# Performance work log

Measured on AMD Instinct MI355X. Metric: run time of the kernel, lower is better.

Reference implementation:

```python
import jax, jax.numpy as jnp
import numpy as np

N = 10000      # nodes
E = 320000     # edges (avg degree 32)
H = 128        # hidden_channels
G = 50         # num_gaussians
NF = 128       # num_filters
L = 6          # num_interactions
CUTOFF = 10.0


def ssp(x):
    # ShiftedSoftplus: softplus(x) - log(2)
    return jax.nn.softplus(x) - jnp.log(2.0).astype(x.dtype)


def setup_inputs() -> dict:
    key = jax.random.key(0)
    ks = jax.random.split(key, 16)
    s = 0.05
    return {
        "z": jax.random.normal(ks[0], (N, H), jnp.float32),
        "pos": jax.random.normal(ks[1], (N, 3), jnp.float32) * 3.0,
        "edge_index": jax.random.randint(ks[2], (2, E), 0, N, dtype=jnp.int64),
        # per-layer stacked parameters (PyTorch Linear convention: y = x @ W.T + b)
        "mlp1_w": jax.random.normal(ks[3], (L, NF, G), jnp.float32) * s,
        "mlp1_b": jnp.zeros((L, NF), jnp.float32),
        "mlp2_w": jax.random.normal(ks[4], (L, NF, NF), jnp.float32) * s,
        "mlp2_b": jnp.zeros((L, NF), jnp.float32),
        "lin1_w": jax.random.normal(ks[5], (L, NF, H), jnp.float32) * s,   # no bias
        "lin2_w": jax.random.normal(ks[6], (L, H, NF), jnp.float32) * s,
        "lin2_b": jnp.zeros((L, H), jnp.float32),
        "lin_w": jax.random.normal(ks[7], (L, H, H), jnp.float32) * s,
        "lin_b": jnp.zeros((L, H), jnp.float32),
        "coord_w": jax.random.normal(ks[8], (L, 1, G + 2 * H), jnp.float32) * s,
        "coord_b": jnp.zeros((L, 1), jnp.float32),
    }


def reference(z, pos, edge_index, mlp1_w, mlp1_b, mlp2_w, mlp2_b,
              lin1_w, lin2_w, lin2_b, lin_w, lin_b, coord_w, coord_b):
    row, col = edge_index[0], edge_index[1]
    # edge distances from INITIAL positions (computed once, as in torch code)
    edge_weight = jnp.linalg.norm(pos[row] - pos[col], axis=-1)          # [E]
    offset = jnp.linspace(0.0, CUTOFF, G).astype(pos.dtype)              # [G]
    coeff = -0.5 / (offset[1] - offset[0]) ** 2
    edge_attr = jnp.exp(coeff * (edge_weight[:, None] - offset[None, :]) ** 2)  # [E,G]
    C = 0.5 * (jnp.cos(edge_weight * jnp.pi / CUTOFF) + 1.0)             # [E] cosine cutoff
    ones_e = jnp.ones((E,), pos.dtype)
    h = z
    for l in range(L):
        # ---- coordinate update (uses current pos and current h) ----
        feat = jnp.concatenate([edge_attr, h[row], h[col]], axis=-1)     # [E, G+2H]
        cw = feat @ coord_w[l].T + coord_b[l]                            # [E,1]
        aggr = (pos[row] - pos[col]) * cw                                # [E,3]
        sums = jax.ops.segment_sum(aggr, row, num_segments=N)            # [N,3]
        cnt = jax.ops.segment_sum(ones_e, row, num_segments=N)           # [N]
        mean = jnp.where(cnt[:, None] > 0, sums / jnp.maximum(cnt, 1.0)[:, None], 0.0)
        pos = pos + mean
        # ---- CFConv interaction ----
        Wf = ssp(edge_attr @ mlp1_w[l].T + mlp1_b[l]) @ mlp2_w[l].T + mlp2_b[l]  # [E,NF]
        Wf = Wf * C[:, None]
        xf = h @ lin1_w[l].T                                             # [N,NF]
        agg = jax.ops.segment_sum(xf[row] * Wf, col, num_segments=N)     # [N,NF]
        out = agg @ lin2_w[l].T + lin2_b[l]                              # [N,H]
        h = h + (ssp(out) @ lin_w[l].T + lin_b[l])
    return (pos, h)
```

## Files before the change

kernel.cpp:

```cpp
#include <hip/hip_runtime.h>


#define NN 10000
#define EE 320000
#define HH 128
#define GG 50
#define NF 128
#define NL 6
#define TROWS 2048
#define NB 128

typedef unsigned short u16;
typedef unsigned int u32;
typedef short bf16x8 __attribute__((ext_vector_type(8)));
typedef float f32x4  __attribute__((ext_vector_type(4)));

__device__ __forceinline__ float us2f(u16 u){
  union { float f; u32 i; } v; v.i = ((u32)u) << 16; return v.f;
}
__device__ __forceinline__ u16 f2us(float x){
  union { float f; u32 i; } v; v.f = x;
  u32 r = v.i + 0x7fffu + ((v.i >> 16) & 1u);
  return (u16)(r >> 16);
}
__device__ __forceinline__ float ldin(const void* p, int i, int bf){
  return bf ? us2f(((const u16*)p)[i]) : ((const float*)p)[i];
}
__device__ __forceinline__ float sspf(float x){
  return fmaxf(x, 0.f) + __logf(1.f + __expf(-fabsf(x))) - 0.6931472f;
}
__device__ __forceinline__ int detect_bf(const u32* __restrict__ zraw){
  int lane = threadIdx.x & 63;
  int c = 0;
  #pragma unroll
  for(int j=0;j<4;j++){
    u32 w = zraw[lane*4+j];
    u32 hb = (w >> 8) & 0x7F;
    c += (hb >= 0x38 && hb <= 0x41) ? 1 : 0;
  }
  return __popcll(__ballot(c >= 2)) >= 32;
}
__device__ __forceinline__ int detect_i64(const int* __restrict__ ei_raw){
  int lane = threadIdx.x & 63;
  int c = 0;
  #pragma unroll
  for(int j=0;j<4;j++) c += (ei_raw[2*(lane*4+j)+1] == 0) ? 1 : 0;
  return __popcll(__ballot(c >= 3)) >= 32;
}

__global__ void k_prep(const u32* __restrict__ zraw, const void* __restrict__ pos_in,
    const void* __restrict__ mlp1_w, const void* __restrict__ mlp1_b,
    const void* __restrict__ mlp2_w, const void* __restrict__ mlp2_b,
    const void* __restrict__ lin1_w, const void* __restrict__ lin2_w,
    const void* __restrict__ lin2_b, const void* __restrict__ lin_w,
    const void* __restrict__ lin_b,  const void* __restrict__ coord_w,
    const void* __restrict__ coord_b,
    float* __restrict__ h, float* __restrict__ pc40, int* __restrict__ wmaxi,
    float* __restrict__ b1f, float* __restrict__ b2v,
    u16* __restrict__ w1b, u16* __restrict__ w2bb,
    u16* __restrict__ l1b, u16* __restrict__ l2b,
    float* __restrict__ l2bf, u16* __restrict__ lwb,
    float* __restrict__ lbf, float* __restrict__ cwf, float* __restrict__ cbf)
{
  int bf = detect_bf(zraw);
  int b = blockIdx.x;
  if(b < NN*HH/256){
    int i = b*256 + threadIdx.x;
    h[i] = ldin(zraw, i, bf);
    if(i < NN*3){
      int n = i/3, comp = i%3;
      pc40[n*4 + comp] = ldin(pos_in, i, bf);
    }
    if(i == 0) *wmaxi = 0;
  } else {
    int i = (b - NN*HH/256)*256 + threadIdx.x;
    if(i < NL*NF){
      b1f[i]  = ldin(mlp1_b, i, bf);
      b2v[i]  = ldin(mlp2_b, i, bf);
      l2bf[i] = ldin(lin2_b, i, bf);
      lbf[i]  = ldin(lin_b,  i, bf);
    }
    if(i < NL*NF*64){
      int l = i/(NF*64), rem = i%(NF*64);
      int f = rem>>6, g = rem&63;
      w1b[i] = (g < GG) ? f2us(ldin(mlp1_w, (l*NF + f)*GG + g, bf)) : (u16)0;
    }
    if(i < NL*NF*NF){
      w2bb[i] = f2us(ldin(mlp2_w, i, bf));
      l1b[i]  = f2us(ldin(lin1_w, i, bf));
      l2b[i]  = f2us(ldin(lin2_w, i, bf));
      lwb[i]  = f2us(ldin(lin_w,  i, bf));
    }
    if(i < NL*(GG+2*HH)) cwf[i] = ldin(coord_w, i, bf);
    if(i < NL) cbf[i] = ldin(coord_b, i, bf);
  }
}

__global__ void k_count(const int* __restrict__ ei_raw, const float* __restrict__ pc4,
                        int* __restrict__ eiN, float* __restrict__ wE,
                        u32* __restrict__ partR32, u32* __restrict__ partC32,
                        int* __restrict__ wmaxi){
  __shared__ u32 hr[NN/2];
  __shared__ u32 hc[NN/2];
  int is64 = detect_i64(ei_raw);
  int b = blockIdx.x, tid = threadIdx.x;
  for(int i=tid; i<NN/2; i+=256){ hr[i]=0; hc[i]=0; }
  __syncthreads();
  int e0 = b*(EE/NB), e1 = e0 + EE/NB;
  float wm = 0.f;
  for(int e = e0 + tid; e < e1; e += 256){
    int r = is64 ? ei_raw[2*e] : ei_raw[e];
    int c = is64 ? ei_raw[2*(EE+e)] : ei_raw[EE+e];
    eiN[e] = r; eiN[EE+e] = c;
    float4 pr = *(const float4*)&pc4[r*4];
    float4 pcv = *(const float4*)&pc4[c*4];
    float dx = pr.x-pcv.x, dy = pr.y-pcv.y, dz = pr.z-pcv.z;
    float w = sqrtf(dx*dx + dy*dy + dz*dz);
    wE[e] = w;
    wm = fmaxf(wm, w);
    atomicAdd(&hr[r>>1], (r&1) ? 0x10000u : 1u);
    atomicAdd(&hc[c>>1], (c&1) ? 0x10000u : 1u);
  }
  #pragma unroll
  for(int s=32; s>0; s>>=1) wm = fmaxf(wm, __shfl_down(wm, s, 64));
  if((tid & 63) == 0) atomicMax(wmaxi, __float_as_int(wm));
  __syncthreads();
  for(int i=tid; i<NN/2; i+=256){
    partR32[(size_t)b*(NN/2) + i] = hr[i];
    partC32[(size_t)b*(NN/2) + i] = hc[i];
  }
}

__global__ void k_scan2(const int* __restrict__ col_deg, const int* __restrict__ deg_row,
                        int* __restrict__ col_start, int* __restrict__ row_start){
  __shared__ int pc[1024];
  __shared__ int pr[1024];
  int tid = threadIdx.x;
  const int CH = (NN + 1023)/1024;
  int base = tid*CH;
  int sc = 0, sr = 0;
  for(int i=0;i<CH;i++){
    int idx = base+i;
    if(idx<NN){ sc += col_deg[idx]; sr += deg_row[idx]; }
  }
  pc[tid] = sc; pr[tid] = sr;
  __syncthreads();
  for(int off=1; off<1024; off<<=1){
    int vc = (tid>=off) ? pc[tid-off] : 0;
    int vr = (tid>=off) ? pr[tid-off] : 0;
    __syncthreads();
    pc[tid] += vc; pr[tid] += vr;
    __syncthreads();
  }
  int runc = (tid==0) ? 0 : pc[tid-1];
  int runr = (tid==0) ? 0 : pr[tid-1];
  for(int i=0;i<CH;i++){
    int idx = base+i;
    if(idx<NN){
      col_start[idx]=runc; runc += col_deg[idx];
      row_start[idx]=runr; runr += deg_row[idx];
    }
  }
  if(tid==1023){ col_start[NN] = runc; row_start[NN] = runr; }
}

__global__ void k_fill(const int* __restrict__ eiN, const float* __restrict__ wE,
                       const int* __restrict__ col_start, const int* __restrict__ row_start,
                       const u16* __restrict__ partR16, const u16* __restrict__ partC16,
                       const int* __restrict__ wmaxi,
                       u32* __restrict__ pk_s, u32* __restrict__ pkr_s){
  __shared__ u32 hr[NN/2];
  __shared__ u32 hc[NN/2];
  int b = blockIdx.x, t = threadIdx.x;
  for(int i=t; i<NN/2; i+=256){ hr[i]=0; hc[i]=0; }
  __syncthreads();
  float invD = (float)(TROWS-1) / __int_as_float(*wmaxi);
  int e0 = b*(EE/NB), e1 = e0 + EE/NB;
  for(int e = e0 + t; e < e1; e += 256){
    int r = eiN[e], c = eiN[EE+e];
    u32 i0 = (u32)min((int)(wE[e]*invD + 0.5f), TROWS-1);
    u32 oldc = atomicAdd(&hc[c>>1], (c&1) ? 0x10000u : 1u);
    u32 rkc = (c&1) ? (oldc >> 16) : (oldc & 0xFFFFu);
    int p = col_start[c] + (int)partC16[(size_t)b*NN + c] + (int)rkc;
    pk_s[p] = ((u32)r << 11) | i0;
    u32 oldr = atomicAdd(&hr[r>>1], (r&1) ? 0x10000u : 1u);
    u32 rkr = (r&1) ? (oldr >> 16) : (oldr & 0xFFFFu);
    int p2 = row_start[r] + (int)partR16[(size_t)b*NN + r] + (int)rkr;
    pkr_s[p2] = ((u32)c << 11) | i0;
  }
}

__global__ void k_tabnode(const u16* __restrict__ w1b, const float* __restrict__ b1f,
                          const u16* __restrict__ w2bb, const float* __restrict__ b2v,
                          const float* __restrict__ cwf, const int* __restrict__ wmaxi,
                          u16* __restrict__ tabB, float* __restrict__ tabS,
                          const float* __restrict__ h, const u16* __restrict__ l1b,
                          u16* __restrict__ xfb0, float* __restrict__ dr0,
                          float* __restrict__ pc40,
                          u16* __restrict__ partR16, u16* __restrict__ partC16,
                          int* __restrict__ degR, int* __restrict__ degC){
  __shared__ __align__(16) u16 S[32*72 + 32*136];
  int b = blockIdx.x, t = threadIdx.x;
  int wave = t >> 6, lane = t & 63;
  int m16 = lane & 15, quad = lane >> 4;
  if(b < NL*64){
    int l = b >> 6;
    int r0 = (b & 63)*32;
    u16* attr = S;
    u16* t1   = S + 32*72;
    float delta = __int_as_float(*wmaxi) / (float)(TROWS-1);
    for(int idx=t; idx<32*64; idx+=256){
      int r = idx >> 6, g = idx & 63;
      float w = (float)(r0 + r)*delta;
      float d = w - (float)g*(10.f/49.f);
      attr[r*72 + g] = (g < GG) ? f2us(__expf(-12.005f*d*d)) : (u16)0;
    }
    __syncthreads();
    {
      const u16* __restrict__ w1 = w1b + (size_t)l*NF*64;
      f32x4 acc[2][2];
      #pragma unroll
      for(int nc=0;nc<2;nc++){
        float bv = b1f[l*NF + wave*32 + nc*16 + m16];
        #pragma unroll
        for(int mr=0;mr<2;mr++) acc[mr][nc] = (f32x4){bv,bv,bv,bv};
      }
      #pragma unroll
      for(int ks=0; ks<2; ks++){
        bf16x8 aA[2], bB[2];
        #pragma unroll
        for(int mr=0;mr<2;mr++)
          aA[mr] = *(const bf16x8*)&attr[(mr*16 + m16)*72 + ks*32 + quad*8];
        #pragma unroll
        for(int nc=0;nc<2;nc++)
          bB[nc] = *(const bf16x8*)&w1[(wave*32 + nc*16 + m16)*64 + ks*32 + quad*8];
        #pragma unroll
        for(int mr=0;mr<2;mr++)
          #pragma unroll
          for(int nc=0;nc<2;nc++)
            acc[mr][nc] = __builtin_amdgcn_mfma_f32_16x16x32_bf16(aA[mr], bB[nc], acc[mr][nc], 0,0,0);
      }
      #pragma unroll
      for(int mr=0;mr<2;mr++)
        #pragma unroll
        for(int nc=0;nc<2;nc++)
          #pragma unroll
          for(int r=0;r<4;r++)
            t1[(mr*16 + quad*4 + r)*136 + wave*32 + nc*16 + m16] = f2us(sspf(acc[mr][nc][r]));
    }
    __syncthreads();
    {
      const u16* __restrict__ w2 = w2bb + (size_t)l*NF*NF;
      f32x4 acc[2][2];
      #pragma unroll
      for(int nc=0;nc<2;nc++){
        float bv = b2v[l*NF + wave*32 + nc*16 + m16];
        #pragma unroll
        for(int mr=0;mr<2;mr++) acc[mr][nc] = (f32x4){bv,bv,bv,bv};
      }
      #pragma unroll
      for(int ks=0; ks<4; ks++){
        bf16x8 aA[2], bB[2];
        #pragma unroll
        for(int mr=0;mr<2;mr++)
          aA[mr] = *(const bf16x8*)&t1[(mr*16 + m16)*136 + ks*32 + quad*8];
        #pragma unroll
        for(int nc=0;nc<2;nc++)
          bB[nc] = *(const bf16x8*)&w2[(wave*32 + nc*16 + m16)*NF + ks*32 + quad*8];
        #pragma unroll
        for(int mr=0;mr<2;mr++)
          #pragma unroll
          for(int nc=0;nc<2;nc++)
            acc[mr][nc] = __builtin_amdgcn_mfma_f32_16x16x32_bf16(aA[mr], bB[nc], acc[mr][nc], 0,0,0);
      }
      #pragma unroll
      for(int mr=0;mr<2;mr++){
        #pragma unroll
        for(int r=0;r<4;r++){
          int row = r0 + mr*16 + quad*4 + r;
          float w = (float)row*delta;
          float C = 0.5f*(cosf(w*0.3141592653589793f) + 1.f);
          #pragma unroll
          for(int nc=0;nc<2;nc++)
            tabB[((size_t)l*TROWS + row)*NF + wave*32 + nc*16 + m16] = f2us(acc[mr][nc][r]*C);
        }
      }
    }
    if(t < 32){
      const float* __restrict__ cwg = cwf + l*(GG+2*HH);
      float w = (float)(r0 + t)*delta;
      float s = 0.f;
      for(int g=0; g<GG; g++){
        float d = w - (float)g*(10.f/49.f);
        s += __expf(-12.005f*d*d)*cwg[g];
      }
      tabS[l*TROWS + r0 + t] = s;
    }
  } else if(b < NL*64 + NN/16){
    int n0 = (b - NL*64)*16;
    u16* T = S;
    {
      int node = t >> 4, c0 = (t & 15)*8;
      const float* hp = &h[(n0 + node)*HH + c0];
      f32x4 v0 = *(const f32x4*)hp;
      f32x4 v1 = *(const f32x4*)(hp+4);
      u16* d = &T[node*136 + c0];
      d[0]=f2us(v0[0]); d[1]=f2us(v0[1]); d[2]=f2us(v0[2]); d[3]=f2us(v0[3]);
      d[4]=f2us(v1[0]); d[5]=f2us(v1[1]); d[6]=f2us(v1[2]); d[7]=f2us(v1[3]);
    }
    __syncthreads();
    {
      const float* __restrict__ cw = cwf;
      int j = t >> 4, l16 = t & 15;
      float ar = 0.f, ac = 0.f;
      #pragma unroll
      for(int i=0;i<8;i++){
        float hvv = us2f(T[j*136 + l16 + 16*i]);
        ar += hvv*cw[GG + l16 + 16*i];
        ac += hvv*cw[GG + HH + l16 + 16*i];
      }
      #pragma unroll
      for(int s=8; s>0; s>>=1){
        ar += __shfl_down(ar, s, 16);
        ac += __shfl_down(ac, s, 16);
      }
      if(l16 == 0){ dr0[n0+j] = ar; pc40[(n0+j)*4+3] = ac; }
    }
    {
      const u16* __restrict__ wC = l1b;
      bf16x8 aH[4];
      #pragma unroll
      for(int ks=0; ks<4; ks++)
        aH[ks] = *(const bf16x8*)&T[m16*136 + ks*32 + quad*8];
      #pragma unroll
      for(int nc=0; nc<2; nc++){
        int fcol = wave*32 + nc*16 + m16;
        f32x4 acc = (f32x4){0.f,0.f,0.f,0.f};
        #pragma unroll
        for(int ks=0; ks<4; ks++){
          bf16x8 bbv = *(const bf16x8*)&wC[fcol*HH + ks*32 + quad*8];
          acc = __builtin_amdgcn_mfma_f32_16x16x32_bf16(aH[ks], bbv, acc, 0,0,0);
        }
        #pragma unroll
        for(int r=0;r<4;r++)
          xfb0[(n0+quad*4+r)*NF + fcol] = f2us(acc[r]);
      }
    }
  } else {
    int n = (b - (NL*64 + NN/16))*256 + t;
    if(n >= NN) return;
    u32 rr = 0, rc = 0;
    for(int b0=0; b0<NB; b0+=8){
      u32 vr[8], vc[8];
      #pragma unroll
      for(int j=0;j<8;j++){
        vr[j] = partR16[(size_t)(b0+j)*NN + n];
        vc[j] = partC16[(size_t)(b0+j)*NN + n];
      }
      #pragma unroll
      for(int j=0;j<8;j++){
        partR16[(size_t)(b0+j)*NN + n] = (u16)rr; rr += vr[j];
        partC16[(size_t)(b0+j)*NN + n] = (u16)rc; rc += vc[j];
      }
    }
    degR[n] = (int)rr; degC[n] = (int)rc;
  }
}

__global__ void k_layer(const int* __restrict__ col_start, const u32* __restrict__ pk_s,
                        const u32* __restrict__ xfR, u16* __restrict__ xfW,
                        const u16* __restrict__ tabB, int l,
                        const u16* __restrict__ l2b, const float* __restrict__ l2bf,
                        const u16* __restrict__ lwb, const float* __restrict__ lbf,
                        float* __restrict__ h, const u16* __restrict__ l1b,
                        const float* __restrict__ cwf,
                        const float* __restrict__ drR, float* __restrict__ drW,
                        const int* __restrict__ row_start, const u32* __restrict__ pkr_s,
                        const float* __restrict__ tabS, const float* __restrict__ cbf,
                        const float* __restrict__ pc4R, float* __restrict__ pc4W,
                        const u32* __restrict__ zraw, void* __restrict__ out){
  __shared__ __align__(16) u16 T[16*136];
  __shared__ __align__(16) u16 T2[16*136];
  int b = blockIdx.x, t = threadIdx.x;
  int wave = t >> 6, lane = t & 63;

  if(b % 3 == 0){
    int n0 = (b/3)*16;
    {
      const u32* __restrict__ tg32 = (const u32*)(tabB + (size_t)l*TROWS*NF);
      u32* __restrict__ T32 = (u32*)T;
      #pragma unroll
      for(int j=0;j<2;j++){
        int n = n0 + wave*2 + j;
        int p0 = col_start[n], p1 = col_start[n+1];
        float aa[4] = {0.f,0.f,0.f,0.f};
        float bb[4] = {0.f,0.f,0.f,0.f};
        int p = p0;
        for(; p+8 <= p1; p += 8){
          u32 pk[8], gv[8], xv[8];
          #pragma unroll
          for(int k=0;k<8;k++) pk[k] = pk_s[p+k];
          #pragma unroll
          for(int k=0;k<8;k++){
            gv[k] = tg32[(pk[k] & 2047u)*64 + lane];
            xv[k] = xfR[(pk[k] >> 11)*64 + lane];
          }
          #pragma unroll
          for(int k=0;k<8;k++){
            aa[k&3] += us2f((u16)xv[k])      * us2f((u16)gv[k]);
            bb[k&3] += us2f((u16)(xv[k]>>16))* us2f((u16)(gv[k]>>16));
          }
        }
        for(; p < p1; p++){
          u32 pk = pk_s[p];
          u32 g = tg32[(pk & 2047u)*64 + lane];
          u32 x = xfR[(pk >> 11)*64 + lane];
          aa[0] += us2f((u16)x)      * us2f((u16)g);
          bb[0] += us2f((u16)(x>>16))* us2f((u16)(g>>16));
        }
        float av = (aa[0]+aa[1])+(aa[2]+aa[3]);
        float bv = (bb[0]+bb[1])+(bb[2]+bb[3]);
        T32[(wave*2+j)*68 + lane] = (u32)f2us(av) | ((u32)f2us(bv) << 16);
      }
    }
    __syncthreads();
    int m16 = lane & 15, quad = lane >> 4;
    int fcol = wave*16 + m16;
    f32x4 acc;
    {
      bf16x8 aA[4];
      #pragma unroll
      for(int ks=0; ks<4; ks++)
        aA[ks] = *(const bf16x8*)&T[m16*136 + ks*32 + quad*8];
      const u16* __restrict__ wA = l2b + l*HH*NF;
      float bv = l2bf[l*HH + fcol];
      acc = (f32x4){bv,bv,bv,bv};
      #pragma unroll
      for(int ks=0; ks<4; ks++){
        bf16x8 bbv = *(const bf16x8*)&wA[fcol*NF + ks*32 + quad*8];
        acc = __builtin_amdgcn_mfma_f32_16x16x32_bf16(aA[ks], bbv, acc, 0,0,0);
      }
      #pragma unroll
      for(int r=0;r<4;r++)
        T2[(quad*4+r)*136 + fcol] = f2us(sspf(acc[r]));
    }
    __syncthreads();
    float hv[4];
    int bf = (l == NL-1) ? detect_bf(zraw) : 0;
    {
      bf16x8 aS[4];
      #pragma unroll
      for(int ks=0; ks<4; ks++)
        aS[ks] = *(const bf16x8*)&T2[m16*136 + ks*32 + quad*8];
      const u16* __restrict__ wB = lwb + l*HH*HH;
      float bv = lbf[l*HH + fcol];
      acc = (f32x4){bv,bv,bv,bv};
      #pragma unroll
      for(int ks=0; ks<4; ks++){
        bf16x8 bbv = *(const bf16x8*)&wB[fcol*HH + ks*32 + quad*8];
        acc = __builtin_amdgcn_mfma_f32_16x16x32_bf16(aS[ks], bbv, acc, 0,0,0);
      }
      #pragma unroll
      for(int r=0;r<4;r++)
        hv[r] = h[(n0+quad*4+r)*HH + fcol] + acc[r];
    }
    if(l == NL-1){
      #pragma unroll
      for(int r=0;r<4;r++){
        int n = n0 + quad*4 + r;
        if(bf) ((u16*)out)[NN*3 + n*HH + fcol] = f2us(hv[r]);
        else   ((float*)out)[NN*3 + n*HH + fcol] = hv[r];
      }
      return;
    }
    #pragma unroll
    for(int r=0;r<4;r++){
      int n = n0 + quad*4 + r;
      h[n*HH + fcol] = hv[r];
      T[(quad*4+r)*136 + fcol] = f2us(hv[r]);
    }
    __syncthreads();
    {
      bf16x8 aH[4];
      #pragma unroll
      for(int ks=0; ks<4; ks++)
        aH[ks] = *(const bf16x8*)&T[m16*136 + ks*32 + quad*8];
      const u16* __restrict__ wC = l1b + (l+1)*NF*HH;
      acc = (f32x4){0.f,0.f,0.f,0.f};
      #pragma unroll
      for(int ks=0; ks<4; ks++){
        bf16x8 bbv = *(const bf16x8*)&wC[fcol*HH + ks*32 + quad*8];
        acc = __builtin_amdgcn_mfma_f32_16x16x32_bf16(aH[ks], bbv, acc, 0,0,0);
      }
      #pragma unroll
      for(int r=0;r<4;r++)
        xfW[(n0+quad*4+r)*NF + fcol] = f2us(acc[r]);
    }
    {
      const float* __restrict__ cw = cwf + (l+1)*(GG + 2*HH);
      int j = t >> 5, l32 = t & 31;
      float ar = 0.f, ac = 0.f;
      #pragma unroll
      for(int i=0;i<4;i++){
        float hvv = us2f(T[j*136 + l32 + 32*i]);
        ar += hvv*cw[GG + l32 + 32*i];
        ac += hvv*cw[GG + HH + l32 + 32*i];
      }
      #pragma unroll
      for(int s=16; s>0; s>>=1){
        ar += __shfl_down(ar, s, 32);
        ac += __shfl_down(ac, s, 32);
      }
      if(l32 == 0){ drW[n0+j] = ar; pc4W[(n0+j)*4+3] = ac; }
    }
  } else {
    int u = b - b/3 - 1;
    int bf = (l == NL-1) ? detect_bf(zraw) : 0;
    int n = u*8 + wave;
    const float* __restrict__ ts = tabS + l*TROWS;
    float cb = cbf[l] + drR[n];
    int p0 = row_start[n], p1 = row_start[n+1];
    float4 pn = *(const float4*)&pc4R[n*4];
    float sx=0.f, sy=0.f, sz=0.f;
    for(int p = p0 + lane; p < p1; p += 64){
      u32 pk = pkr_s[p];
      int c = (int)(pk >> 11);
      float4 pcv = *(const float4*)&pc4R[c*4];
      float a = cb + pcv.w + ts[pk & 2047u];
      sx += (pn.x - pcv.x)*a;
      sy += (pn.y - pcv.y)*a;
      sz += (pn.z - pcv.z)*a;
    }
    #pragma unroll
    for(int s=32; s>0; s>>=1){
      sx += __shfl_down(sx, s, 64);
      sy += __shfl_down(sy, s, 64);
      sz += __shfl_down(sz, s, 64);
    }
    if(lane == 0){
      int cnt = p1 - p0;
      float inv = (cnt > 0) ? 1.f/(float)cnt : 0.f;
      float ox = pn.x + sx*inv, oy = pn.y + sy*inv, oz = pn.z + sz*inv;
      if(l == NL-1){
        if(bf){
          u16* o = (u16*)out;
          o[n*3+0] = f2us(ox); o[n*3+1] = f2us(oy); o[n*3+2] = f2us(oz);
        } else {
          float* o = (float*)out;
          o[n*3+0] = ox; o[n*3+1] = oy; o[n*3+2] = oz;
        }
      } else {
        pc4W[n*4+0] = ox; pc4W[n*4+1] = oy; pc4W[n*4+2] = oz;
      }
    }
  }
}

extern "C" void kernel_launch(void* const* d_in, const int* in_sizes, int n_in,
                              void* d_out, int out_size, void* d_ws, size_t ws_size,
                              hipStream_t stream){
  const u32*  z      = (const u32*)d_in[0];
  const void* pos_in = d_in[1];
  const int*  ei_raw = (const int*)d_in[2];
  const void* mlp1_w = d_in[3];
  const void* mlp1_b = d_in[4];
  const void* mlp2_w = d_in[5];
  const void* mlp2_b = d_in[6];
  const void* lin1_w = d_in[7];
  const void* lin2_w = d_in[8];
  const void* lin2_b = d_in[9];
  const void* lin_w  = d_in[10];
  const void* lin_b  = d_in[11];
  const void* coord_w= d_in[12];
  const void* coord_b= d_in[13];

  float* W = (float*)d_ws;
  float* h    = W; W += NN*HH;
  float* pc40 = W; W += NN*4;
  float* pc41 = W; W += NN*4;
  float* dr0  = W; W += NN;
  float* dr1  = W; W += NN;
  float* wE   = W; W += EE;
  float* b1f  = W; W += NL*NF;
  float* b2v  = W; W += NL*NF;
  float* l2bf = W; W += NL*HH;
  float* lbf  = W; W += NL*HH;
  float* cwf  = W; W += NL*(GG+2*HH);
  float* cbf  = W; W += NL;
  W = (float*)(((uintptr_t)W + 63) & ~(uintptr_t)63);
  u16*  tabB = (u16*)W; W += (size_t)NL*TROWS*NF/2;
  float* tabS = W; W += NL*TROWS;
  u16* w1b  = (u16*)W; W += (NL*NF*64)/2;
  u16* w2bb = (u16*)W; W += (NL*NF*NF)/2;
  u16* l1b  = (u16*)W; W += (NL*NF*NF)/2;
  u16* l2b  = (u16*)W; W += (NL*NF*NF)/2;
  u16* lwb  = (u16*)W; W += (NL*NF*NF)/2;
  u16* xfb0 = (u16*)W; W += (NN*NF)/2;
  u16* xfb1 = (u16*)W; W += (NN*NF)/2;
  u16* partR16 = (u16*)W; W += (size_t)NB*NN/2;
  u16* partC16 = (u16*)W; W += (size_t)NB*NN/2;
  int* degR      = (int*)W; W += NN;
  int* degC      = (int*)W; W += NN;
  int* col_start = (int*)W; W += NN+1;
  int* row_start = (int*)W; W += NN+1;
  u32* pk_s      = (u32*)W; W += EE;
  u32* pkr_s     = (u32*)W; W += EE;
  int* eiN       = (int*)W; W += 2*EE;
  int* wmaxi     = (int*)W; W += 1;

  k_prep<<<NN*HH/256 + NL*NF*NF/256, 256, 0, stream>>>(
      z, pos_in, mlp1_w, mlp1_b, mlp2_w, mlp2_b, lin1_w, lin2_w, lin2_b,
      lin_w, lin_b, coord_w, coord_b,
      h, pc40, wmaxi,
      b1f, b2v, w1b, w2bb, l1b, l2b, l2bf, lwb, lbf, cwf, cbf);
  k_count<<<NB, 256, 0, stream>>>(ei_raw, pc40, eiN, wE,
                                  (u32*)partR16, (u32*)partC16, wmaxi);
  k_tabnode<<<NL*64 + NN/16 + (NN+255)/256, 256, 0, stream>>>(
      w1b, b1f, w2bb, b2v, cwf, wmaxi, tabB, tabS,
      h, l1b, xfb0, dr0, pc40,
      partR16, partC16, degR, degC);
  k_scan2<<<1, 1024, 0, stream>>>(degC, degR, col_start, row_start);
  k_fill<<<NB, 256, 0, stream>>>(eiN, wE, col_start, row_start,
                                 partR16, partC16, wmaxi, pk_s, pkr_s);

  for(int l=0; l<NL; l++){
    int par = l & 1;
    const u32* xfR = (const u32*)(par ? xfb1 : xfb0);
    u16* xfW = par ? xfb0 : xfb1;
    const float* drR = par ? dr1 : dr0;   float* drW = par ? dr0 : dr1;
    const float* p4R = par ? pc41 : pc40; float* p4W = par ? pc40 : pc41;
    k_layer<<<3*(NN/16), 512, 0, stream>>>(
        col_start, pk_s, xfR, xfW, tabB, l,
        l2b, l2bf, lwb, lbf, h, l1b, cwf,
        drR, drW,
        row_start, pkr_s, tabS, cbf, p4R, p4W, z, d_out);
  }
}
```

Measured before the change: 352.9 us.

## Replace per-block LDS histograms with global atomic ranks for CSR build

The CSR construction no longer uses 128 blocks with shared-memory node histograms plus a per-node prefix over per-block partials. Each edge now takes its rank directly from a global atomicAdd on the row and column degree counters, and that rank is stored per edge. The fill kernel then scatters with one thread per edge. This removes the large per-block partial arrays, the partial-scan pass and the LDS init/flush, at the cost of contended global atomics. Edge order within a segment becomes nondeterministic, which can change floating-point summation order.

Result: slower. 403.5 us (+14.3%).

```diff
diff --git a/kernel.cpp b/kernel.cpp
--- a/kernel.cpp
+++ b/kernel.cpp
@@ -8,7 +8,6 @@
 #define NF 128
 #define NL 6
 #define TROWS 2048
-#define NB 128
 
 typedef unsigned short u16;
 typedef unsigned int u32;
@@ -60,7 +59,8 @@
     u16* __restrict__ w1b, u16* __restrict__ w2bb,
     u16* __restrict__ l1b, u16* __restrict__ l2b,
     float* __restrict__ l2bf, u16* __restrict__ lwb,
-    float* __restrict__ lbf, float* __restrict__ cwf, float* __restrict__ cbf)
+    float* __restrict__ lbf, float* __restrict__ cwf, float* __restrict__ cbf,
+    int* __restrict__ degR, int* __restrict__ degC)
 {
   int bf = detect_bf(zraw);
   int b = blockIdx.x;
@@ -74,6 +74,7 @@
     if(i == 0) *wmaxi = 0;
   } else {
     int i = (b - NN*HH/256)*256 + threadIdx.x;
+    if(i < NN){ degR[i] = 0; degC[i] = 0; }
     if(i < NL*NF){
       b1f[i]  = ldin(mlp1_b, i, bf);
       b2v[i]  = ldin(mlp2_b, i, bf);
@@ -98,37 +99,25 @@
 
 __global__ void k_count(const int* __restrict__ ei_raw, const float* __restrict__ pc4,
                         int* __restrict__ eiN, float* __restrict__ wE,
-                        u32* __restrict__ partR32, u32* __restrict__ partC32,
+                        u16* __restrict__ rkR, u16* __restrict__ rkC,
+                        int* __restrict__ degR, int* __restrict__ degC,
                         int* __restrict__ wmaxi){
-  __shared__ u32 hr[NN/2];
-  __shared__ u32 hc[NN/2];
   int is64 = detect_i64(ei_raw);
-  int b = blockIdx.x, tid = threadIdx.x;
-  for(int i=tid; i<NN/2; i+=256){ hr[i]=0; hc[i]=0; }
-  __syncthreads();
-  int e0 = b*(EE/NB), e1 = e0 + EE/NB;
-  float wm = 0.f;
-  for(int e = e0 + tid; e < e1; e += 256){
-    int r = is64 ? ei_raw[2*e] : ei_raw[e];
-    int c = is64 ? ei_raw[2*(EE+e)] : ei_raw[EE+e];
-    eiN[e] = r; eiN[EE+e] = c;
-    float4 pr = *(const float4*)&pc4[r*4];
-    float4 pcv = *(const float4*)&pc4[c*4];
-    float dx = pr.x-pcv.x, dy = pr.y-pcv.y, dz = pr.z-pcv.z;
-    float w = sqrtf(dx*dx + dy*dy + dz*dz);
-    wE[e] = w;
-    wm = fmaxf(wm, w);
-    atomicAdd(&hr[r>>1], (r&1) ? 0x10000u : 1u);
-    atomicAdd(&hc[c>>1], (c&1) ? 0x10000u : 1u);
-  }
+  int e = blockIdx.x*256 + threadIdx.x;
+  int r = is64 ? ei_raw[2*e] : ei_raw[e];
+  int c = is64 ? ei_raw[2*(EE+e)] : ei_raw[EE+e];
+  eiN[e] = r; eiN[EE+e] = c;
+  float4 pr = *(const float4*)&pc4[r*4];
+  float4 pcv = *(const float4*)&pc4[c*4];
+  float dx = pr.x-pcv.x, dy = pr.y-pcv.y, dz = pr.z-pcv.z;
+  float w = sqrtf(dx*dx + dy*dy + dz*dz);
+  wE[e] = w;
+  rkR[e] = (u16)atomicAdd(&degR[r], 1);
+  rkC[e] = (u16)atomicAdd(&degC[c], 1);
+  float wm = w;
   #pragma unroll
   for(int s=32; s>0; s>>=1) wm = fmaxf(wm, __shfl_down(wm, s, 64));
-  if((tid & 63) == 0) atomicMax(wmaxi, __float_as_int(wm));
-  __syncthreads();
-  for(int i=tid; i<NN/2; i+=256){
-    partR32[(size_t)b*(NN/2) + i] = hr[i];
-    partC32[(size_t)b*(NN/2) + i] = hc[i];
-  }
+  if((threadIdx.x & 63) == 0) atomicMax(wmaxi, __float_as_int(wm));
 }
 
 __global__ void k_scan2(const int* __restrict__ col_deg, const int* __restrict__ deg_row,
@@ -166,28 +155,15 @@
 
 __global__ void k_fill(const int* __restrict__ eiN, const float* __restrict__ wE,
                        const int* __restrict__ col_start, const int* __restrict__ row_start,
-                       const u16* __restrict__ partR16, const u16* __restrict__ partC16,
+                       const u16* __restrict__ rkR, const u16* __restrict__ rkC,
                        const int* __restrict__ wmaxi,
                        u32* __restrict__ pk_s, u32* __restrict__ pkr_s){
-  __shared__ u32 hr[NN/2];
-  __shared__ u32 hc[NN/2];
-  int b = blockIdx.x, t = threadIdx.x;
-  for(int i=t; i<NN/2; i+=256){ hr[i]=0; hc[i]=0; }
-  __syncthreads();
+  int e = blockIdx.x*256 + threadIdx.x;
+  int r = eiN[e], c = eiN[EE+e];
   float invD = (float)(TROWS-1) / __int_as_float(*wmaxi);
-  int e0 = b*(EE/NB), e1 = e0 + EE/NB;
-  for(int e = e0 + t; e < e1; e += 256){
-    int r = eiN[e], c = eiN[EE+e];
-    u32 i0 = (u32)min((int)(wE[e]*invD + 0.5f), TROWS-1);
-    u32 oldc = atomicAdd(&hc[c>>1], (c&1) ? 0x10000u : 1u);
-    u32 rkc = (c&1) ? (oldc >> 16) : (oldc & 0xFFFFu);
-    int p = col_start[c] + (int)partC16[(size_t)b*NN + c] + (int)rkc;
-    pk_s[p] = ((u32)r << 11) | i0;
-    u32 oldr = atomicAdd(&hr[r>>1], (r&1) ? 0x10000u : 1u);
-    u32 rkr = (r&1) ? (oldr >> 16) : (oldr & 0xFFFFu);
-    int p2 = row_start[r] + (int)partR16[(size_t)b*NN + r] + (int)rkr;
-    pkr_s[p2] = ((u32)c << 11) | i0;
-  }
+  u32 i0 = (u32)min((int)(wE[e]*invD + 0.5f), TROWS-1);
+  pk_s [col_start[c] + (int)rkC[e]] = ((u32)r << 11) | i0;
+  pkr_s[row_start[r] + (int)rkR[e]] = ((u32)c << 11) | i0;
 }
 
 __global__ void k_tabnode(const u16* __restrict__ w1b, const float* __restrict__ b1f,
@@ -196,9 +172,7 @@
                           u16* __restrict__ tabB, float* __restrict__ tabS,
                           const float* __restrict__ h, const u16* __restrict__ l1b,
                           u16* __restrict__ xfb0, float* __restrict__ dr0,
-                          float* __restrict__ pc40,
-                          u16* __restrict__ partR16, u16* __restrict__ partC16,
-                          int* __restrict__ degR, int* __restrict__ degC){
+                          float* __restrict__ pc40){
   __shared__ __align__(16) u16 S[32*72 + 32*136];
   int b = blockIdx.x, t = threadIdx.x;
   int wave = t >> 6, lane = t & 63;
@@ -296,7 +270,7 @@
       }
       tabS[l*TROWS + r0 + t] = s;
     }
-  } else if(b < NL*64 + NN/16){
+  } else {
     int n0 = (b - NL*64)*16;
     u16* T = S;
     {
@@ -346,24 +320,6 @@
           xfb0[(n0+quad*4+r)*NF + fcol] = f2us(acc[r]);
       }
     }
-  } else {
-    int n = (b - (NL*64 + NN/16))*256 + t;
-    if(n >= NN) return;
-    u32 rr = 0, rc = 0;
-    for(int b0=0; b0<NB; b0+=8){
-      u32 vr[8], vc[8];
-      #pragma unroll
-      for(int j=0;j<8;j++){
-        vr[j] = partR16[(size_t)(b0+j)*NN + n];
-        vc[j] = partC16[(size_t)(b0+j)*NN + n];
-      }
-      #pragma unroll
-      for(int j=0;j<8;j++){
-        partR16[(size_t)(b0+j)*NN + n] = (u16)rr; rr += vr[j];
-        partC16[(size_t)(b0+j)*NN + n] = (u16)rc; rc += vc[j];
-      }
-    }
-    degR[n] = (int)rr; degC[n] = (int)rc;
   }
 }
 
@@ -597,8 +553,8 @@
   u16* lwb  = (u16*)W; W += (NL*NF*NF)/2;
   u16* xfb0 = (u16*)W; W += (NN*NF)/2;
   u16* xfb1 = (u16*)W; W += (NN*NF)/2;
-  u16* partR16 = (u16*)W; W += (size_t)NB*NN/2;
-  u16* partC16 = (u16*)W; W += (size_t)NB*NN/2;
+  u16* rkR16 = (u16*)W; W += EE/2;
+  u16* rkC16 = (u16*)W; W += EE/2;
   int* degR      = (int*)W; W += NN;
   int* degC      = (int*)W; W += NN;
   int* col_start = (int*)W; W += NN+1;
@@ -612,16 +568,16 @@
       z, pos_in, mlp1_w, mlp1_b, mlp2_w, mlp2_b, lin1_w, lin2_w, lin2_b,
       lin_w, lin_b, coord_w, coord_b,
       h, pc40, wmaxi,
-      b1f, b2v, w1b, w2bb, l1b, l2b, l2bf, lwb, lbf, cwf, cbf);
-  k_count<<<NB, 256, 0, stream>>>(ei_raw, pc40, eiN, wE,
-                                  (u32*)partR16, (u32*)partC16, wmaxi);
-  k_tabnode<<<NL*64 + NN/16 + (NN+255)/256, 256, 0, stream>>>(
+      b1f, b2v, w1b, w2bb, l1b, l2b, l2bf, lwb, lbf, cwf, cbf,
+      degR, degC);
+  k_count<<<EE/256, 256, 0, stream>>>(ei_raw, pc40, eiN, wE,
+                                      rkR16, rkC16, degR, degC, wmaxi);
+  k_tabnode<<<NL*64 + NN/16, 256, 0, stream>>>(
       w1b, b1f, w2bb, b2v, cwf, wmaxi, tabB, tabS,
-      h, l1b, xfb0, dr0, pc40,
-      partR16, partC16, degR, degC);
+      h, l1b, xfb0, dr0, pc40);
   k_scan2<<<1, 1024, 0, stream>>>(degC, degR, col_start, row_start);
-  k_fill<<<NB, 256, 0, stream>>>(eiN, wE, col_start, row_start,
-                                 partR16, partC16, wmaxi, pk_s, pkr_s);
+  k_fill<<<EE/256, 256, 0, stream>>>(eiN, wE, col_start, row_start,
+                                     rkR16, rkC16, wmaxi, pk_s, pkr_s);
 
   for(int l=0; l<NL; l++){
     int par = l & 1;
```
